# Optimization experiments

Measured on AMD Instinct MI355X. Metric: run time of the kernel, lower is better.

Reference implementation:

```python
import jax, jax.numpy as jnp
import numpy as np

B, N, K, CIN, COUT, H = 4, 2048, 32, 16, 32, 32
EPS = 1e-5


def setup_inputs() -> dict:
    key = jax.random.key(0)
    ks = jax.random.split(key, 6)
    s = 0.1
    return dict(
        xyz=jax.random.uniform(ks[0], (B, N, 3), dtype=jnp.float32),
        points=jax.random.normal(ks[1], (B, N, CIN), dtype=jnp.float32),
        W1=jax.random.normal(ks[2], (3, H), dtype=jnp.float32) * s,
        b1=jnp.zeros((H,), jnp.float32),
        g1=jnp.ones((H,), jnp.float32),
        be1=jnp.zeros((H,), jnp.float32),
        W2=jax.random.normal(ks[3], (H, H), dtype=jnp.float32) * s,
        b2=jnp.zeros((H,), jnp.float32),
        g2=jnp.ones((H,), jnp.float32),
        be2=jnp.zeros((H,), jnp.float32),
        W3=jax.random.normal(ks[4], (H, CIN * COUT), dtype=jnp.float32) * s,
        b3=jnp.zeros((CIN * COUT,), jnp.float32),
        gbn=jnp.ones((COUT,), jnp.float32),
        bbn=jnp.zeros((COUT,), jnp.float32),
    )


def _bn(h, g, b):
    # BatchNorm1d training-mode math: biased batch stats over axis 0
    return g * (h - h.mean(0)) / jnp.sqrt(h.var(0) + EPS) + b


def reference(xyz, points, W1, b1, g1, be1, W2, b2, g2, be2, W3, b3, gbn, bbn):
    # KNN: squared distances (B,N,N)
    sq = jnp.sum(xyz * xyz, -1)
    dist = -2.0 * jnp.einsum('bmc,bnc->bmn', xyz, xyz) + sq[:, :, None] + sq[:, None, :]
    _, idx = jax.lax.top_k(-dist, K)  # (B,N,K) nearest neighbors

    gather = jax.vmap(lambda p, i: p[i])  # (N,C),(N,K)->(N,K,C), vmapped over B
    grouped_xyz = gather(xyz, idx)                      # (B,N,K,3)
    rel = grouped_xyz - xyz[:, :, None, :]              # (B,N,K,3)
    grouped_pts = gather(points, idx)                   # (B,N,K,CIN)

    # weight net on relative coords
    h = rel.reshape(-1, 3)
    h = _bn(jax.nn.relu(h @ W1 + b1), g1, be1)
    h = _bn(jax.nn.relu(h @ W2 + b2), g2, be2)
    w = (h @ W3 + b3).reshape(B, N, K, CIN, COUT)       # (B,N,K,CIN,COUT)

    # weighted sum over C_in, then max over neighbors
    out = jnp.einsum('bnkc,bnkco->bnko', grouped_pts, w)  # (B,N,K,COUT)
    out = out.max(axis=2)                                 # (B,N,COUT)

    # final BatchNorm1d over (B,N) per channel
    m = out.mean((0, 1))
    v = out.var((0, 1))
    return gbn * (out - m) / jnp.sqrt(v + EPS) + bbn
```

## Files before the change

kernel.cpp:

```cpp
#include <hip/hip_runtime.h>

#define B_ 4
#define N_ 2048
#define K_ 32
#define CIN_ 16
#define COUT_ 32
#define H_ 32
#define R_ (B_*N_*K_)
#define EPS_ 1e-5f
#define INVR_ (1.0f/(float)R_)
#define INVBN_ (1.0f/(float)(B_*N_))
#define LISTCAP 160
#define NSH 16

typedef __attribute__((ext_vector_type(8)))  _Float16 f16x8;
typedef __attribute__((ext_vector_type(2)))  __fp16   hw16x2;
typedef __attribute__((ext_vector_type(2)))  _Float16 f16x2;
typedef __attribute__((ext_vector_type(16))) float    f32x16;

__device__ __forceinline__ float dot3f(float ax,float ay,float az,float bx,float by,float bz){
    return fmaf(az,bz, fmaf(ay,by, ax*bx));
}
__device__ __forceinline__ unsigned int pk2(float a, float b){
    union { hw16x2 v; unsigned int u; } c;
    c.v = __builtin_amdgcn_cvt_pkrtz(a, b);
    return c.u;
}
__device__ __forceinline__ unsigned int pkmul(unsigned int a, unsigned int b){
    union { unsigned int u; f16x2 v; } x, y, r;
    x.u = a; y.u = b; r.v = x.v * y.v; return r.u;
}
__device__ __forceinline__ float shsum(const float* __restrict__ p, int k){
    float s = 0.f;
    #pragma unroll
    for (int i = 0; i < NSH; ++i) s += p[i*32 + k];
    return s;
}

__global__ __launch_bounds__(256,3) void k_knn(const float* __restrict__ xyz,
                                               const float* __restrict__ W1, const float* __restrict__ b1,
                                               int* __restrict__ idx_out,
                                               float* __restrict__ s1sh, float* __restrict__ q1sh,
                                               unsigned int* __restrict__ h1f){
    __shared__ float4 sp[N_];
    __shared__ unsigned int hist[4][512];
    __shared__ unsigned long long lst[4][LISTCAP];
    __shared__ int kidx[4][K_];

    const int tid  = threadIdx.x;
    const int w    = tid >> 6;
    const int lane = tid & 63;
    const int half = lane >> 5;
    const int b    = blockIdx.x >> 9;
    const int q    = ((blockIdx.x & 511) << 2) + w;
    const int bN   = b * N_;
    unsigned int* hw = &hist[w][0];

    {
        const float* xb = xyz + (size_t)bN*3;
        #pragma unroll
        for (int pt = tid; pt < N_; pt += 256){
            float x = xb[3*pt], y = xb[3*pt+1], z = xb[3*pt+2];
            sp[pt] = make_float4(x, y, z, dot3f(x,y,z,x,y,z));
        }
    }

    {
        const uint4 z4 = make_uint4(0,0,0,0);
        uint4* h4 = (uint4*)hw;
        h4[lane] = z4; h4[64 + lane] = z4;
    }
    __syncthreads();

    const float4 qp = sp[q];
    const float qx = qp.x, qy = qp.y, qz = qp.z, sqq = qp.w;

    unsigned int fv[32];
    #pragma unroll
    for (int j = 0; j < 32; ++j){
        int c = j*64 + lane;
        float4 pt = sp[c];
        float d = fmaf(-2.0f, dot3f(qx,qy,qz, pt.x,pt.y,pt.z), sqq) + pt.w;
        fv[j] = __float_as_uint(d);
        unsigned int u1 = __float_as_uint(d + 1.0f);
        unsigned int key = (u1 <= 0x3F800000u) ? 0u : ((u1 - 0x3F800000u) >> 15);
        key = key > 511u ? 511u : key;
        atomicAdd(&hw[key], 1u);
    }

    unsigned int g[8];
    {
        uint4 h0 = ((const uint4*)hw)[lane*2];
        uint4 h1u = ((const uint4*)hw)[lane*2 + 1];
        g[0]=h0.x; g[1]=h0.y; g[2]=h0.z; g[3]=h0.w;
        g[4]=h1u.x; g[5]=h1u.y; g[6]=h1u.z; g[7]=h1u.w;
    }
    unsigned int gs = 0;
    #pragma unroll
    for (int t = 0; t < 8; ++t) gs += g[t];
    unsigned int cum = gs;
    #pragma unroll
    for (int off = 1; off < 64; off <<= 1){
        unsigned int v = __shfl_up(cum, off);
        if (lane >= off) cum += v;
    }
    unsigned long long bal = __ballot(cum >= (unsigned)K_);
    int L = __ffsll(bal) - 1;
    unsigned int run = __shfl(cum, L) - __shfl(gs, L);
    int Bsel = 8*L + 7;
    {
        unsigned int c = run; bool fnd = false;
        #pragma unroll
        for (int t = 0; t < 8; ++t){
            unsigned int ht = __shfl(g[t], L, 64);
            if (!fnd && c + ht >= (unsigned)K_){ Bsel = 8*L + t; fnd = true; }
            c += ht;
        }
    }
    const float Tedge = __uint_as_float(0x3F800000u + ((unsigned)(Bsel + 1) << 15));
    const bool allin = (Bsel == 511);

    const unsigned long long mlt = (lane == 63) ? ~0ull >> 1 : (1ull << lane) - 1ull;
    unsigned int cnt = 0;
    #pragma unroll
    for (int j = 0; j < 32; ++j){
        float f1 = __uint_as_float(fv[j]) + 1.0f;
        bool surv = (f1 < Tedge) || allin;
        unsigned long long sb = __ballot(surv);
        unsigned int pos = cnt + (unsigned int)__popcll(sb & mlt);
        if (surv && pos < (unsigned)LISTCAP)
            lst[w][pos] = ((unsigned long long)fv[j] << 32) | (unsigned int)(j*64 + lane);
        cnt += (unsigned int)__popcll(sb);
    }
    int m = (int)cnt; if (m > LISTCAP) m = LISTCAP;

    int* outp = idx_out + ((size_t)bN + q) * K_;
    for (int i = lane; i < m; i += 64){
        unsigned long long my = lst[w][i];
        int rank = 0;
        int jj = 0;
        for (; jj + 8 <= m; jj += 8){
            const ulonglong2* pv = (const ulonglong2*)&lst[w][jj];
            ulonglong2 v0 = pv[0], v1 = pv[1], v2 = pv[2], v3 = pv[3];
            rank += (int)(v0.x < my) + (int)(v0.y < my) + (int)(v1.x < my) + (int)(v1.y < my)
                  + (int)(v2.x < my) + (int)(v2.y < my) + (int)(v3.x < my) + (int)(v3.y < my);
        }
        for (; jj < m; ++jj) rank += (lst[w][jj] < my) ? 1 : 0;
        if (rank < K_){
            int id = (int)(unsigned int)(my & 0xFFFFFFFFull);
            outp[rank] = id;
            kidx[w][rank] = id;
        }
    }

    {
        const int ch = lane & 31;
        float w1a = W1[ch], w1b = W1[H_+ch], w1c = W1[2*H_+ch], b1c = b1[ch];
        float s = 0.f, qq = 0.f;
        #pragma unroll
        for (int r = 0; r < 16; ++r){
            int idr = kidx[w][half*16 + r];
            float4 pn = sp[idr];
            float rx = pn.x - qx, ry = pn.y - qy, rz = pn.z - qz;
            float h = fmaxf(fmaf(rx, w1a, fmaf(ry, w1b, fmaf(rz, w1c, b1c))), 0.0f);
            s += h; qq = fmaf(h, h, qq);
        }
        s  += __shfl_xor(s, 32, 64);
        qq += __shfl_xor(qq, 32, 64);
        if (lane < 32){
            int sh = (blockIdx.x & (NSH-1)) * 32 + ch;
            atomicAdd(&s1sh[sh], s);
            atomicAdd(&q1sh[sh], qq);
        }
    }

    {
        const int id = kidx[w][lane & 31];
        float4 pn = sp[id];
        float rx = pn.x - qx, ry = pn.y - qy, rz = pn.z - qz;
        uint4* dst = (uint4*)h1f + (size_t)(bN + q)*128 + lane;
        const int c0 = half*8;
        #pragma unroll
        for (int sblk = 0; sblk < 2; ++sblk){
            const int cb = sblk*16 + c0;
            const float4 wa0 = *(const float4*)(W1 + cb);
            const float4 wa1 = *(const float4*)(W1 + cb + 4);
            const float4 wb0 = *(const float4*)(W1 + H_ + cb);
            const float4 wb1 = *(const float4*)(W1 + H_ + cb + 4);
            const float4 wc0 = *(const float4*)(W1 + 2*H_ + cb);
            const float4 wc1 = *(const float4*)(W1 + 2*H_ + cb + 4);
            const float4 bv0 = *(const float4*)(b1 + cb);
            const float4 bv1 = *(const float4*)(b1 + cb + 4);
            float h0 = fmaxf(fmaf(rx, wa0.x, fmaf(ry, wb0.x, fmaf(rz, wc0.x, bv0.x))), 0.0f);
            float h1v= fmaxf(fmaf(rx, wa0.y, fmaf(ry, wb0.y, fmaf(rz, wc0.y, bv0.y))), 0.0f);
            float h2v= fmaxf(fmaf(rx, wa0.z, fmaf(ry, wb0.z, fmaf(rz, wc0.z, bv0.z))), 0.0f);
            float h3 = fmaxf(fmaf(rx, wa0.w, fmaf(ry, wb0.w, fmaf(rz, wc0.w, bv0.w))), 0.0f);
            float h4 = fmaxf(fmaf(rx, wa1.x, fmaf(ry, wb1.x, fmaf(rz, wc1.x, bv1.x))), 0.0f);
            float h5 = fmaxf(fmaf(rx, wa1.y, fmaf(ry, wb1.y, fmaf(rz, wc1.y, bv1.y))), 0.0f);
            float h6 = fmaxf(fmaf(rx, wa1.z, fmaf(ry, wb1.z, fmaf(rz, wc1.z, bv1.z))), 0.0f);
            float h7 = fmaxf(fmaf(rx, wa1.w, fmaf(ry, wb1.w, fmaf(rz, wc1.w, bv1.w))), 0.0f);
            uint4 o;
            o.x = pk2(h0, h1v); o.y = pk2(h2v, h3); o.z = pk2(h4, h5); o.w = pk2(h6, h7);
            dst[sblk*64] = o;
        }
    }
}

__device__ __forceinline__ void build_l2(const float* __restrict__ s1s, const float* __restrict__ q1s,
                                         const float* __restrict__ g1, const float* __restrict__ be1,
                                         const float* __restrict__ W2, const float* __restrict__ b2,
                                         float* a1L, float* bb1L, unsigned int* W2L, float* b2pL,
                                         int tid){
    if (tid < H_){
        float s = shsum(s1s, tid), qq = shsum(q1s, tid);
        float mm = s*INVR_, vv = qq*INVR_ - mm*mm;
        float aa = g1[tid] / sqrtf(vv + EPS_);
        a1L[tid]  = aa;
        bb1L[tid] = fmaf(-aa, mm, be1[tid]);
    }
    __syncthreads();
    #pragma unroll
    for (int e = 0; e < 2; ++e){
        int d = tid*2 + e;
        int jj = d & 3, ln = (d >> 2) & 63, s = d >> 8;
        int col = ln & 31;
        int k0 = s*16 + ((ln >> 5) << 3) + 2*jj;
        W2L[d] = pk2(a1L[k0]*W2[k0*H_ + col], a1L[k0+1]*W2[(k0+1)*H_ + col]);
    }
    if (tid < H_){
        float acc = b2[tid];
        #pragma unroll 4
        for (int h = 0; h < H_; ++h) acc = fmaf(bb1L[h], W2[h*H_ + tid], acc);
        b2pL[tid] = acc;
    }
}

__global__ __launch_bounds__(256,4) void k_h2stats(const uint4* __restrict__ h1f,
                                                   const float* __restrict__ points, unsigned int* __restrict__ pf16,
                                                   const float* __restrict__ s1s, const float* __restrict__ q1s,
                                                   const float* __restrict__ g1, const float* __restrict__ be1,
                                                   const float* __restrict__ W2, const float* __restrict__ b2,
                                                   float* s2s, float* q2s){
    __shared__ float redS[H_], redQ[H_];
    __shared__ float a1L[H_], bb1L[H_], b2pL[H_];
    __shared__ unsigned int W2L[512];
    const int tid = threadIdx.x, lane = tid & 63, w = tid >> 6;
    const int m = lane & 31;
    {
        int pp = blockIdx.x*256 + tid;
        if (pp < 65536) pf16[pp] = pk2(points[2*pp], points[2*pp+1]);
    }
    if (tid < H_){ redS[tid] = 0.f; redQ[tid] = 0.f; }
    build_l2(s1s, q1s, g1, be1, W2, b2, a1L, bb1L, W2L, b2pL, tid);
    __syncthreads();

    union { uint4 u4; f16x8 v; } Bf0, Bf1;
    Bf0.u4 = ((const uint4*)W2L)[lane];
    Bf1.u4 = ((const uint4*)W2L)[64 + lane];
    float b2c = b2pL[m];
    const int blk0 = blockIdx.x*16 + w*4;

    float s = 0.f, q = 0.f;
    #pragma unroll
    for (int t = 0; t < 4; ++t){
        union { uint4 u4; f16x8 v; } a0, a1f;
        a0.u4  = h1f[(size_t)(blk0 + t)*128 + lane];
        a1f.u4 = h1f[(size_t)(blk0 + t)*128 + 64 + lane];
        f32x16 acc;
        #pragma unroll
        for (int i = 0; i < 16; ++i) acc[i] = b2c;
        acc = __builtin_amdgcn_mfma_f32_32x32x16_f16(a0.v,  Bf0.v, acc, 0, 0, 0);
        acc = __builtin_amdgcn_mfma_f32_32x32x16_f16(a1f.v, Bf1.v, acc, 0, 0, 0);
        #pragma unroll
        for (int i = 0; i < 16; ++i){
            float v = fmaxf(acc[i], 0.0f);
            s += v; q = fmaf(v, v, q);
        }
    }
    s += __shfl_xor(s, 32, 64);
    q += __shfl_xor(q, 32, 64);
    if (lane < 32){ atomicAdd(&redS[m], s); atomicAdd(&redQ[m], q); }
    __syncthreads();
    if (tid < H_){
        int sh = (blockIdx.x & (NSH-1)) * 32 + tid;
        atomicAdd(&s2s[sh], redS[tid]);
        atomicAdd(&q2s[sh], redQ[tid]);
    }
}

#define PHASEA(T, H2P, GSEL) do { \
    union { uint4 u4; f16x8 v; } B0f, B1f; \
    B0f.u4 = h1f[(size_t)(blk0 + (T))*128 + lane]; \
    B1f.u4 = h1f[(size_t)(blk0 + (T))*128 + 64 + lane]; \
    int row = rB + (T)*32 + m; \
    int bb_ = row >> 16; \
    int idr = idx[row]; \
    const uint4* gpp = (const uint4*)(pf16 + ((size_t)bb_*N_ + idr)*8); \
    uint4 ga = gpp[0], gb = gpp[1]; \
    GSEL[0] = half ? gb.x : ga.x; \
    GSEL[1] = half ? gb.y : ga.y; \
    GSEL[2] = half ? gb.z : ga.z; \
    GSEL[3] = half ? gb.w : ga.w; \
    f32x16 c2; \
    _Pragma("unroll") \
    for (int i = 0; i < 16; ++i) c2[i] = b2v[i]; \
    c2 = __builtin_amdgcn_mfma_f32_32x32x16_f16(A0.v, B0f.v, c2, 0, 0, 0); \
    c2 = __builtin_amdgcn_mfma_f32_32x32x16_f16(A1.v, B1f.v, c2, 0, 0, 0); \
    _Pragma("unroll") \
    for (int p = 0; p < 8; ++p){ \
        float v0 = fmaxf(c2[2*p],   0.0f); \
        float v1 = fmaxf(c2[2*p+1], 0.0f); \
        unsigned int ow = pk2(v0, v1); \
        unsigned int ot = __shfl_xor(ow, 32, 64); \
        int a = p >> 1, bb = p & 1; \
        H2P[4*a + bb]     = half ? ot : ow; \
        H2P[4*a + 2 + bb] = half ? ow : ot; \
    } \
} while(0)

#define REDST(ACC, T) do { \
    float v = ACC[0]; \
    _Pragma("unroll") \
    for (int i = 1; i < 16; ++i) v = fmaxf(v, ACC[i]); \
    v = fmaxf(v, __shfl_xor(v, 32, 64)); \
    if (lane < 32){ \
        int g = blk0 + (T); \
        out_pre[(size_t)g*COUT_ + m] = v; \
        atomicAdd(&redS[m], v); \
        atomicAdd(&redQ[m], v*v); \
    } \
} while(0)

__global__ __launch_bounds__(256,4) void k_out(const uint4* __restrict__ h1f, const int* __restrict__ idx,
                                               const float* __restrict__ s1s, const float* __restrict__ q1s,
                                               const float* __restrict__ g1, const float* __restrict__ be1,
                                               const float* __restrict__ W2, const float* __restrict__ b2,
                                               const float* __restrict__ s2s, const float* __restrict__ q2s,
                                               const float* __restrict__ g2, const float* __restrict__ be2,
                                               const float* __restrict__ W3, const float* __restrict__ b3,
                                               const unsigned int* __restrict__ pf16,
                                               float* __restrict__ out_pre, float* s3s, float* q3s){
    __shared__ uint4 Wls[2112];
    __shared__ float redS[COUT_], redQ[COUT_];
    __shared__ float a1L[H_], bb1L[H_], b2pL[H_], aa2L[H_], bb2L[H_];
    __shared__ unsigned int W2L[512];
    const int tid = threadIdx.x, lane = tid & 63, w = tid >> 6;
    const int half = lane >> 5, m = lane & 31;
    if (tid < COUT_){
        redS[tid] = 0.f; redQ[tid] = 0.f;
        float ss = shsum(s2s, tid), qq = shsum(q2s, tid);
        float mm = ss*INVR_, vv = qq*INVR_ - mm*mm;
        float aa = g2[tid] / sqrtf(vv + EPS_);
        aa2L[tid] = aa;
        bb2L[tid] = fmaf(-aa, mm, be2[tid]);
    }
    build_l2(s1s, q1s, g1, be1, W2, b2, a1L, bb1L, W2L, b2pL, tid);
    {
        int jj = tid & 3, ln = tid >> 2;
        int col = ln & 31, c0 = ((ln >> 5) << 3) + 2*jj;
        unsigned int* WlsD = (unsigned int*)Wls;
        #pragma unroll 4
        for (int i = 0; i < 32; ++i){
            float a = aa2L[i];
            WlsD[i*256 + tid] = pk2(a*W3[i*512 + c0*COUT_ + col], a*W3[i*512 + (c0+1)*COUT_ + col]);
        }
        float v0 = b3[c0*COUT_ + col], v1 = b3[(c0+1)*COUT_ + col];
        #pragma unroll 4
        for (int h = 0; h < H_; ++h){
            v0 = fmaf(bb2L[h], W3[h*512 + c0*COUT_ + col], v0);
            v1 = fmaf(bb2L[h], W3[h*512 + (c0+1)*COUT_ + col], v1);
        }
        WlsD[32*256 + tid] = pk2(v0, v1);
    }
    __syncthreads();

    const int rB = blockIdx.x*256 + w*64;
    const int blk0 = blockIdx.x*8 + w*2;

    union { uint4 u4; f16x8 v; } A0, A1;
    A0.u4 = ((const uint4*)W2L)[lane];
    A1.u4 = ((const uint4*)W2L)[64 + lane];
    float b2v[16];
    #pragma unroll
    for (int i = 0; i < 16; ++i) b2v[i] = b2pL[(i&3) + 8*(i>>2) + 4*half];

    unsigned int h2p0[16], h2p1[16];
    unsigned int gsel0[4], gsel1[4];
    PHASEA(0, h2p0, gsel0);
    PHASEA(1, h2p1, gsel1);

    f32x16 acc0, acc1;
    #pragma unroll
    for (int i = 0; i < 16; ++i){ acc0[i] = 0.f; acc1[i] = 0.f; }
    #pragma unroll
    for (int kb = 0; kb < 32; ++kb){
        union { uint4 u4; f16x8 v; } bf; bf.u4 = Wls[kb*64 + lane];
        const unsigned int sel = (kb & 1) ? 0x03020302u : 0x01000100u;
        unsigned int hr0 = h2p0[kb >> 1];
        unsigned int hd0 = __builtin_amdgcn_perm(hr0, hr0, sel);
        union { unsigned int u[4]; f16x8 v; } af;
        #pragma unroll
        for (int jj = 0; jj < 4; ++jj) af.u[jj] = pkmul(hd0, gsel0[jj]);
        acc0 = __builtin_amdgcn_mfma_f32_32x32x16_f16(af.v, bf.v, acc0, 0, 0, 0);
        unsigned int hr1 = h2p1[kb >> 1];
        unsigned int hd1 = __builtin_amdgcn_perm(hr1, hr1, sel);
        #pragma unroll
        for (int jj = 0; jj < 4; ++jj) af.u[jj] = pkmul(hd1, gsel1[jj]);
        acc1 = __builtin_amdgcn_mfma_f32_32x32x16_f16(af.v, bf.v, acc1, 0, 0, 0);
    }
    {
        union { uint4 u4; f16x8 v; } bf; bf.u4 = Wls[32*64 + lane];
        union { unsigned int u[4]; f16x8 v; } af;
        #pragma unroll
        for (int jj = 0; jj < 4; ++jj) af.u[jj] = gsel0[jj];
        acc0 = __builtin_amdgcn_mfma_f32_32x32x16_f16(af.v, bf.v, acc0, 0, 0, 0);
        #pragma unroll
        for (int jj = 0; jj < 4; ++jj) af.u[jj] = gsel1[jj];
        acc1 = __builtin_amdgcn_mfma_f32_32x32x16_f16(af.v, bf.v, acc1, 0, 0, 0);
    }

    REDST(acc0, 0);
    REDST(acc1, 1);

    __syncthreads();
    if (tid < COUT_){
        int sh = (blockIdx.x & (NSH-1)) * 32 + tid;
        atomicAdd(&s3s[sh], redS[tid]);
        atomicAdd(&q3s[sh], redQ[tid]);
    }
}

__global__ __launch_bounds__(256) void k_bn(const float4* __restrict__ out_pre4,
                                            const float* __restrict__ s3s, const float* __restrict__ q3s,
                                            const float* __restrict__ gbn, const float* __restrict__ bbn,
                                            float4* __restrict__ out4){
    __shared__ float aaL[COUT_], bbL[COUT_];
    const int tid = threadIdx.x;
    if (tid < COUT_){
        float ss = shsum(s3s, tid), qq = shsum(q3s, tid);
        float mm = ss*INVBN_, vv = qq*INVBN_ - mm*mm;
        float aa = gbn[tid]/sqrtf(vv + EPS_);
        aaL[tid] = aa;
        bbL[tid] = fmaf(-aa, mm, bbn[tid]);
    }
    __syncthreads();
    int i = blockIdx.x*256 + tid;
    int o = (i*4) & (COUT_-1);
    float4 v = out_pre4[i];
    float4 r;
    r.x = fmaf(aaL[o],   v.x, bbL[o]);
    r.y = fmaf(aaL[o+1], v.y, bbL[o+1]);
    r.z = fmaf(aaL[o+2], v.z, bbL[o+2]);
    r.w = fmaf(aaL[o+3], v.w, bbL[o+3]);
    out4[i] = r;
}

extern "C" void kernel_launch(void* const* d_in, const int* in_sizes, int n_in,
                              void* d_out, int out_size, void* d_ws, size_t ws_size,
                              hipStream_t stream){
    const float* xyz    = (const float*)d_in[0];
    const float* points = (const float*)d_in[1];
    const float* W1  = (const float*)d_in[2];
    const float* b1  = (const float*)d_in[3];
    const float* g1  = (const float*)d_in[4];
    const float* be1 = (const float*)d_in[5];
    const float* W2  = (const float*)d_in[6];
    const float* b2  = (const float*)d_in[7];
    const float* g2  = (const float*)d_in[8];
    const float* be2 = (const float*)d_in[9];
    const float* W3  = (const float*)d_in[10];
    const float* b3  = (const float*)d_in[11];
    const float* gbn = (const float*)d_in[12];
    const float* bbn = (const float*)d_in[13];
    float* out = (float*)d_out;

    char* base = (char*)d_ws;
    int*            idx     = (int*)(base + 0);
    float*          out_pre = (float*)(base + 1048576);
    unsigned int*   pf16    = (unsigned int*)(base + 2097152);
    float*          st      = (float*)(base + 2359296);
    unsigned int*   h1f     = (unsigned int*)(base + 4194304);
    float *s1s=st, *q1s=st+512, *s2s=st+1024, *q2s=st+1536, *s3s=st+2048, *q3s=st+2560;

    hipMemsetAsync((void*)st, 0, 12288, stream);

    hipLaunchKernelGGL(k_knn,     dim3(B_*N_/4),  dim3(256), 0, stream, xyz, W1, b1, idx, s1s, q1s, h1f);
    hipLaunchKernelGGL(k_h2stats, dim3(R_/512),   dim3(256), 0, stream, (const uint4*)h1f,
                       points, pf16, s1s, q1s, g1, be1, W2, b2, s2s, q2s);
    hipLaunchKernelGGL(k_out,     dim3(R_/256),   dim3(256), 0, stream, (const uint4*)h1f, idx,
                       s1s, q1s, g1, be1, W2, b2, s2s, q2s, g2, be2, W3, b3, pf16, out_pre, s3s, q3s);
    hipLaunchKernelGGL(k_bn,      dim3(256),      dim3(256), 0, stream, (const float4*)out_pre, s3s, q3s,
                       gbn, bbn, (float4*)out);
}
```

Baseline: 156.2 us.

## Halve k_out grid, process four point tiles per wave, stage W3 via LDS

Each k_out block now handles 512 rows (four 32-point tiles per wave over two loop passes), so the per-block weight preparation of the scaled W3 matrix is paid across twice the work. The W3 preload is restructured to copy coalesced float4 chunks into a new 16 KB shared buffer in four groups, and the scaled-weight and bias folding are computed in one combined pass. This costs extra shared memory and barriers, and occupancy drops to 3 blocks per CU, with half as many blocks to spread across the device.

```diff
diff --git a/kernel.cpp b/kernel.cpp
--- a/kernel.cpp
+++ b/kernel.cpp
@@ -331,7 +331,7 @@
     } \
 } while(0)
 
-__global__ __launch_bounds__(256,4) void k_out(const uint4* __restrict__ h1f, const int* __restrict__ idx,
+__global__ __launch_bounds__(256,3) void k_out(const uint4* __restrict__ h1f, const int* __restrict__ idx,
                                                const float* __restrict__ s1s, const float* __restrict__ q1s,
                                                const float* __restrict__ g1, const float* __restrict__ be1,
                                                const float* __restrict__ W2, const float* __restrict__ b2,
@@ -341,6 +341,7 @@
                                                const unsigned int* __restrict__ pf16,
                                                float* __restrict__ out_pre, float* s3s, float* q3s){
     __shared__ uint4 Wls[2112];
+    __shared__ float w3s[4096];
     __shared__ float redS[COUT_], redQ[COUT_];
     __shared__ float a1L[H_], bb1L[H_], b2pL[H_], aa2L[H_], bb2L[H_];
     __shared__ unsigned int W2L[512];
@@ -357,25 +358,34 @@
     build_l2(s1s, q1s, g1, be1, W2, b2, a1L, bb1L, W2L, b2pL, tid);
     {
         int jj = tid & 3, ln = tid >> 2;
-        int col = ln & 31, c0 = ((ln >> 5) << 3) + 2*jj;
+        int col = ln & 31;
+        int c0 = ((ln >> 5) << 3) + 2*jj;
+        const int e0 = c0*COUT_ + col, e1 = e0 + COUT_;
         unsigned int* WlsD = (unsigned int*)Wls;
-        #pragma unroll 4
-        for (int i = 0; i < 32; ++i){
-            float a = aa2L[i];
-            WlsD[i*256 + tid] = pk2(a*W3[i*512 + c0*COUT_ + col], a*W3[i*512 + (c0+1)*COUT_ + col]);
-        }
-        float v0 = b3[c0*COUT_ + col], v1 = b3[(c0+1)*COUT_ + col];
-        #pragma unroll 4
-        for (int h = 0; h < H_; ++h){
-            v0 = fmaf(bb2L[h], W3[h*512 + c0*COUT_ + col], v0);
-            v1 = fmaf(bb2L[h], W3[h*512 + (c0+1)*COUT_ + col], v1);
-        }
-        WlsD[32*256 + tid] = pk2(v0, v1);
-    }
-    __syncthreads();
-
-    const int rB = blockIdx.x*256 + w*64;
-    const int blk0 = blockIdx.x*8 + w*2;
+        float bv0 = b3[e0], bv1 = b3[e1];
+        #pragma unroll 1
+        for (int grp = 0; grp < 4; ++grp){
+            const float4* src = (const float4*)(W3 + grp*4096);
+            #pragma unroll
+            for (int u = 0; u < 4; ++u)
+                ((float4*)w3s)[u*256 + tid] = src[u*256 + tid];
+            __syncthreads();
+            #pragma unroll
+            for (int r = 0; r < 8; ++r){
+                int i = grp*8 + r;
+                float v0 = w3s[r*512 + e0], v1 = w3s[r*512 + e1];
+                WlsD[i*256 + tid] = pk2(aa2L[i]*v0, aa2L[i]*v1);
+                bv0 = fmaf(bb2L[i], v0, bv0);
+                bv1 = fmaf(bb2L[i], v1, bv1);
+            }
+            __syncthreads();
+        }
+        WlsD[32*256 + tid] = pk2(bv0, bv1);
+    }
+    __syncthreads();
+
+    const int blk0 = blockIdx.x*16 + w*4;
+    const int rB   = blk0*32;
 
     union { uint4 u4; f16x8 v; } A0, A1;
     A0.u4 = ((const uint4*)W2L)[lane];
@@ -384,43 +394,46 @@
     #pragma unroll
     for (int i = 0; i < 16; ++i) b2v[i] = b2pL[(i&3) + 8*(i>>2) + 4*half];
 
-    unsigned int h2p0[16], h2p1[16];
-    unsigned int gsel0[4], gsel1[4];
-    PHASEA(0, h2p0, gsel0);
-    PHASEA(1, h2p1, gsel1);
-
-    f32x16 acc0, acc1;
-    #pragma unroll
-    for (int i = 0; i < 16; ++i){ acc0[i] = 0.f; acc1[i] = 0.f; }
-    #pragma unroll
-    for (int kb = 0; kb < 32; ++kb){
-        union { uint4 u4; f16x8 v; } bf; bf.u4 = Wls[kb*64 + lane];
-        const unsigned int sel = (kb & 1) ? 0x03020302u : 0x01000100u;
-        unsigned int hr0 = h2p0[kb >> 1];
-        unsigned int hd0 = __builtin_amdgcn_perm(hr0, hr0, sel);
-        union { unsigned int u[4]; f16x8 v; } af;
-        #pragma unroll
-        for (int jj = 0; jj < 4; ++jj) af.u[jj] = pkmul(hd0, gsel0[jj]);
-        acc0 = __builtin_amdgcn_mfma_f32_32x32x16_f16(af.v, bf.v, acc0, 0, 0, 0);
-        unsigned int hr1 = h2p1[kb >> 1];
-        unsigned int hd1 = __builtin_amdgcn_perm(hr1, hr1, sel);
-        #pragma unroll
-        for (int jj = 0; jj < 4; ++jj) af.u[jj] = pkmul(hd1, gsel1[jj]);
-        acc1 = __builtin_amdgcn_mfma_f32_32x32x16_f16(af.v, bf.v, acc1, 0, 0, 0);
-    }
-    {
-        union { uint4 u4; f16x8 v; } bf; bf.u4 = Wls[32*64 + lane];
-        union { unsigned int u[4]; f16x8 v; } af;
-        #pragma unroll
-        for (int jj = 0; jj < 4; ++jj) af.u[jj] = gsel0[jj];
-        acc0 = __builtin_amdgcn_mfma_f32_32x32x16_f16(af.v, bf.v, acc0, 0, 0, 0);
-        #pragma unroll
-        for (int jj = 0; jj < 4; ++jj) af.u[jj] = gsel1[jj];
-        acc1 = __builtin_amdgcn_mfma_f32_32x32x16_f16(af.v, bf.v, acc1, 0, 0, 0);
-    }
-
-    REDST(acc0, 0);
-    REDST(acc1, 1);
+    #pragma unroll 1
+    for (int tp = 0; tp < 2; ++tp){
+        unsigned int h2p0[16], h2p1[16];
+        unsigned int gsel0[4], gsel1[4];
+        PHASEA(2*tp,     h2p0, gsel0);
+        PHASEA(2*tp + 1, h2p1, gsel1);
+
+        f32x16 acc0, acc1;
+        #pragma unroll
+        for (int i = 0; i < 16; ++i){ acc0[i] = 0.f; acc1[i] = 0.f; }
+        #pragma unroll
+        for (int kb = 0; kb < 32; ++kb){
+            union { uint4 u4; f16x8 v; } bf; bf.u4 = Wls[kb*64 + lane];
+            const unsigned int sel = (kb & 1) ? 0x03020302u : 0x01000100u;
+            unsigned int hr0 = h2p0[kb >> 1];
+            unsigned int hd0 = __builtin_amdgcn_perm(hr0, hr0, sel);
+            union { unsigned int u[4]; f16x8 v; } af;
+            #pragma unroll
+            for (int jj = 0; jj < 4; ++jj) af.u[jj] = pkmul(hd0, gsel0[jj]);
+            acc0 = __builtin_amdgcn_mfma_f32_32x32x16_f16(af.v, bf.v, acc0, 0, 0, 0);
+            unsigned int hr1 = h2p1[kb >> 1];
+            unsigned int hd1 = __builtin_amdgcn_perm(hr1, hr1, sel);
+            #pragma unroll
+            for (int jj = 0; jj < 4; ++jj) af.u[jj] = pkmul(hd1, gsel1[jj]);
+            acc1 = __builtin_amdgcn_mfma_f32_32x32x16_f16(af.v, bf.v, acc1, 0, 0, 0);
+        }
+        {
+            union { uint4 u4; f16x8 v; } bf; bf.u4 = Wls[32*64 + lane];
+            union { unsigned int u[4]; f16x8 v; } af;
+            #pragma unroll
+            for (int jj = 0; jj < 4; ++jj) af.u[jj] = gsel0[jj];
+            acc0 = __builtin_amdgcn_mfma_f32_32x32x16_f16(af.v, bf.v, acc0, 0, 0, 0);
+            #pragma unroll
+            for (int jj = 0; jj < 4; ++jj) af.u[jj] = gsel1[jj];
+            acc1 = __builtin_amdgcn_mfma_f32_32x32x16_f16(af.v, bf.v, acc1, 0, 0, 0);
+        }
+
+        REDST(acc0, 2*tp);
+        REDST(acc1, 2*tp + 1);
+    }
 
     __syncthreads();
     if (tid < COUT_){
@@ -487,7 +500,7 @@
     hipLaunchKernelGGL(k_knn,     dim3(B_*N_/4),  dim3(256), 0, stream, xyz, W1, b1, idx, s1s, q1s, h1f);
     hipLaunchKernelGGL(k_h2stats, dim3(R_/512),   dim3(256), 0, stream, (const uint4*)h1f,
                        points, pf16, s1s, q1s, g1, be1, W2, b2, s2s, q2s);
-    hipLaunchKernelGGL(k_out,     dim3(R_/256),   dim3(256), 0, stream, (const uint4*)h1f, idx,
+    hipLaunchKernelGGL(k_out,     dim3(R_/512),   dim3(256), 0, stream, (const uint4*)h1f, idx,
                        s1s, q1s, g1, be1, W2, b2, s2s, q2s, g2, be2, W3, b3, pf16, out_pre, s3s, q3s);
     hipLaunchKernelGGL(k_bn,      dim3(256),      dim3(256), 0, stream, (const float4*)out_pre, s3s, q3s,
                        gbn, bbn, (float4*)out);
```

After: 159.4 us. 2.1% more time.
